# Kernel tuning notes

Hardware: AMD Instinct MI355X
Metric: run time of the kernel (lower is better)

## Reference

```python
import jax, jax.numpy as jnp
import numpy as np

# NSA hyperparams (match init_kwargs)
D_BLK = 64    # d: block stride
L_CMP = 64    # compression block length (== d -> non-overlapping blocks)
L_SLC = 64    # selection block length (== l_cmp == d -> P_slc = P_cmp)
BQ = 64       # block_size_q
TOPK = 16     # slc_top_k
WL, WR = 512, 0  # sliding window (left, right)


def _nsa_forward(q, k, v, w_k, b_k, w_v, b_v, w_gate, b_gate, seqlen):
    S, qh, dim = q.shape
    kv = k.shape[1]
    H = qh // kv
    b = S // seqlen          # number of equal-length packed sequences
    s = seqlen
    scale = dim ** -0.5
    f32 = jnp.float32

    # [b, s, kv, H, e]: q head g*H+h belongs to kv head g (repeat_interleave layout)
    q5 = q.reshape(b, s, kv, H, dim)
    k3 = k.reshape(b, s, kv, dim)
    v3 = v.reshape(b, s, kv, dim)

    # ---- block compression (extract_blocks + cmp_linear over block length) ----
    n_blk = s // D_BLK
    kb = k.reshape(b, n_blk, D_BLK, kv, dim)
    vb = v.reshape(b, n_blk, D_BLK, kv, dim)
    K_cmp = jnp.einsum('bntke,t->bnke', kb, w_k) + b_k[0]
    V_cmp = jnp.einsum('bntke,t->bnke', vb, w_v) + b_v[0]

    # ---- compressed attention (per sequence, fp32 softmax) ----
    sc = jnp.einsum('bqkhe,bnke->bkhqn', q5, K_cmp).astype(f32) * scale
    P = jax.nn.softmax(sc, axis=-1)
    out_cmp = jnp.einsum('bkhqn,bnke->bqkhe', P.astype(q.dtype), V_cmp)

    # ---- selection scores: pool P over q-blocks and GQA groups, then top-k ----
    nqb = s // BQ
    pooled = P.reshape(b, kv, H, nqb, BQ, n_blk).sum(axis=(2, 4))  # [b,kv,nqb,n_blk]
    idx = jax.lax.top_k(pooled, TOPK)[1]                            # [b,kv,nqb,TOPK]

    # gather selected K/V blocks (shared by all queries in a q-block / GQA group)
    kb2 = jnp.transpose(kb, (0, 3, 1, 2, 4))  # [b,kv,n_blk,l,e]
    vb2 = jnp.transpose(vb, (0, 3, 1, 2, 4))
    gather = jax.vmap(jax.vmap(lambda blocks, i: blocks[i]))
    K_sel = gather(kb2, idx)  # [b,kv,nqb,TOPK,l,e]
    V_sel = gather(vb2, idx)

    # ---- selected-block attention ----
    qblk = q5.reshape(b, nqb, BQ, kv, H, dim)
    sc2 = jnp.einsum('bnckhe,bkntle->bkhnctl', qblk, K_sel).astype(f32) * scale
    sc2 = sc2.reshape(b, kv, H, nqb, BQ, TOPK * L_SLC)
    P2 = jax.nn.softmax(sc2, axis=-1).astype(q.dtype)
    out_slc = jnp.einsum('bkhncm,bknme->bnckhe', P2,
                         V_sel.reshape(b, kv, nqb, TOPK * L_SLC, dim))
    out_slc = out_slc.reshape(b, s, kv, H, dim)

    # ---- sliding-window attention (window_size=(WL, WR), non-causal flag) ----
    sw = jnp.einsum('bikhe,bjke->bkhij', q5, k3).astype(f32) * scale
    i = jnp.arange(s)[:, None]
    j = jnp.arange(s)[None, :]
    valid = (j >= i - WL) & (j <= i + WR)
    sw = jnp.where(valid, sw, -jnp.inf)
    Pw = jax.nn.softmax(sw, axis=-1).astype(q.dtype)
    out_win = jnp.einsum('bkhij,bjke->bikhe', Pw, v3)

    # ---- gated fusion of the three branches ----
    gate = jax.nn.sigmoid(jnp.einsum('bqkhe,ec->bqkhc', q5, w_gate) + b_gate)
    out = (gate[..., 0:1] * out_cmp
           + gate[..., 1:2] * out_slc
           + gate[..., 2:3] * out_win)
    return out.reshape(S, qh, dim)


def setup_inputs() -> dict:
    key = jax.random.key(0)
    ks = jax.random.split(key, 9)
    S, qh, kvh, dim = 4096, 8, 2, 128
    inp = {
        'q': jax.random.normal(ks[0], (S, qh, dim), jnp.float32),
        'k': jax.random.normal(ks[1], (S, kvh, dim), jnp.float32),
        'v': jax.random.normal(ks[2], (S, kvh, dim), jnp.float32),
        'w_k': jax.random.normal(ks[3], (L_CMP,), jnp.float32) * (L_CMP ** -0.5),
        'b_k': jax.random.normal(ks[4], (1,), jnp.float32) * 0.02,
        'w_v': jax.random.normal(ks[5], (L_CMP,), jnp.float32) * (L_CMP ** -0.5),
        'b_v': jax.random.normal(ks[6], (1,), jnp.float32) * 0.02,
        'w_gate': jax.random.normal(ks[7], (dim, 3), jnp.float32) * (dim ** -0.5),
        'b_gate': jax.random.normal(ks[8], (3,), jnp.float32) * 0.02,
        'seqlen': 2048,
    }
    return inp


def reference(q, k, v, w_k, b_k, w_v, b_v, w_gate, b_gate, seqlen):
    return _nsa_forward(q, k, v, w_k, b_k, w_v, b_v, w_gate, b_gate, seqlen)
```

## Files before the change

### kernel.cpp

```cpp
#include <hip/hip_runtime.h>
#include <hip/hip_bf16.h>


#define SEQ   2048
#define NB    2
#define KV    2
#define NH    4
#define QH    8
#define DIM   128
#define NBLK  32
#define NQB   32
#define NTOP  16
#define SCALE 0.08838834764831845f
#define QSC   0.12751831795244785f
#define QS    36
#define RS    144
#define PLS   33
#define VP    72

typedef unsigned short ushort_t;
using bf16x8 = __attribute__((ext_vector_type(8))) short;
using f32x4  = __attribute__((ext_vector_type(4))) float;

__device__ __forceinline__ unsigned pkbf(float a, float b){
  union { __hip_bfloat162 h; unsigned u; } cv;
  cv.h = __float22bfloat162_rn(make_float2(a, b));
  return cv.u;
}

__device__ __forceinline__ void async16(ushort_t* l, const ushort_t* g){
  __builtin_amdgcn_global_load_lds(
      (const __attribute__((address_space(1))) unsigned int*)(size_t)g,
      (__attribute__((address_space(3))) unsigned int*)(size_t)l,
      16, 0, 0);
}

__global__ __launch_bounds__(256) void prep_k(
    const float* __restrict__ k, const float* __restrict__ v,
    const float* __restrict__ w_k, const float* __restrict__ b_k,
    const float* __restrict__ w_v, const float* __restrict__ b_v,
    ushort_t* __restrict__ Kb, ushort_t* __restrict__ VT,
    float* __restrict__ Kc, float* __restrict__ Vc)
{
  int blk = blockIdx.x;
  int db = blk & 1, rb = (blk >> 1) & 31, bbg = blk >> 6;
  int bb = bbg >> 1, g = bbg & 1;
  int tid = threadIdx.x;
  __shared__ ushort_t T[64*VP];
  __shared__ float wks[64], wvs[64];
  __shared__ float accK[16][64], accV[16][64];

  if (tid < 64){ wks[tid] = w_k[tid]; wvs[tid] = w_v[tid]; }
  __syncthreads();

  float4 sk = {0,0,0,0}, sv = {0,0,0,0};
  for (int jj = 0; jj < 4; ++jj){
    int i = tid + jj*256;
    int r = i >> 4, ds = i & 15;
    size_t src = ((size_t)(bb*SEQ + rb*64 + r)*KV + g)*DIM + db*64 + ds*4;
    float4 kx = *(const float4*)(k + src);
    float4 vx = *(const float4*)(v + src);
    uint2 kk; kk.x = pkbf(kx.x,kx.y); kk.y = pkbf(kx.z,kx.w);
    size_t rowb = ((size_t)bbg*SEQ + rb*64 + r)*DIM*2;
    int swz = (db*128 + ds*8) ^ ((r & 7) << 4);
    *(uint2*)((char*)Kb + rowb + swz) = kk;
    unsigned v01 = pkbf(vx.x,vx.y), v23 = pkbf(vx.z,vx.w);
    T[(ds*4+0)*VP + r] = (ushort_t)(v01 & 0xffffu);
    T[(ds*4+1)*VP + r] = (ushort_t)(v01 >> 16);
    T[(ds*4+2)*VP + r] = (ushort_t)(v23 & 0xffffu);
    T[(ds*4+3)*VP + r] = (ushort_t)(v23 >> 16);
    float a = wks[r], b = wvs[r];
    sk.x += a*kx.x; sk.y += a*kx.y; sk.z += a*kx.z; sk.w += a*kx.w;
    sv.x += b*vx.x; sv.y += b*vx.y; sv.z += b*vx.z; sv.w += b*vx.w;
  }
  *(float4*)&accK[tid>>4][(tid&15)*4] = sk;
  *(float4*)&accV[tid>>4][(tid&15)*4] = sv;
  __syncthreads();

  for (int jj = 0; jj < 4; ++jj){
    int i = tid + jj*256;
    int d = i >> 4, seg = i & 15;
    uint2 u = *(uint2*)&T[d*VP + seg*4];
    size_t rowb = ((size_t)bbg*DIM + db*64 + d)*SEQ*2;
    int swz = (seg*8) ^ ((d & 7) << 4);
    *(uint2*)((char*)VT + rowb + rb*128 + swz) = u;
  }

  size_t obase = ((size_t)(bbg*NBLK + rb))*DIM + db*64;
  if (tid < 64){
    float s = 0.f;
#pragma unroll
    for (int i = 0; i < 16; ++i) s += accK[i][tid];
    Kc[obase + tid] = s + b_k[0];
  } else if (tid < 128){
    int d = tid - 64;
    float s = 0.f;
#pragma unroll
    for (int i = 0; i < 16; ++i) s += accV[i][d];
    Vc[obase + d] = s + b_v[0];
  }
}

__global__ __launch_bounds__(256) void cmp_attn_k(
    const float* __restrict__ q, const float* __restrict__ Kc,
    const float* __restrict__ Vc,
    const float* __restrict__ w_gate, const float* __restrict__ b_gate,
    float* __restrict__ pooled_part, float* __restrict__ out)
{
  int blk = blockIdx.x;
  int h  = blk & 3;
  int qb = (blk >> 2) & (NQB-1);
  int g  = (blk >> 7) & 1;
  int bb = blk >> 8;
  int tid = threadIdx.x;
  int qi = tid >> 2, c = tid & 3;

  __shared__ float Ks[32*RS];
  __shared__ float Vs[32*RS];
  __shared__ float Pl[64*PLS];

  const float4* Ksrc = (const float4*)(Kc + (size_t)(bb*KV + g) * NBLK * DIM);
  const float4* Vsrc = (const float4*)(Vc + (size_t)(bb*KV + g) * NBLK * DIM);
  for (int i = tid; i < 1024; i += 256){
    int row = i >> 5, seg = i & 31;
    int dst = row*RS + (seg>>3)*QS + (seg&7)*4;
    ((float4*)(Ks+dst))[0] = Ksrc[i];
    ((float4*)(Vs+dst))[0] = Vsrc[i];
  }
  __syncthreads();

  int row = bb*SEQ + qb*64 + qi;
  const float* qptr = q + ((size_t)row*QH + g*NH + h)*DIM;

  float sc[8];
#pragma unroll
  for (int nn = 0; nn < 8; ++nn) sc[nn] = 0.f;
  float gp = 0.f;
  for (int qq = 0; qq < 4; ++qq){
    float qv[32];
    const float4* q4 = (const float4*)(qptr + qq*32);
#pragma unroll
    for (int j = 0; j < 8; ++j){
      float4 u = q4[j];
      qv[4*j+0]=u.x; qv[4*j+1]=u.y; qv[4*j+2]=u.z; qv[4*j+3]=u.w;
    }
#pragma unroll
    for (int d = 0; d < 32; ++d) gp += qv[d]*w_gate[(qq*32+d)*3 + 0];
#pragma unroll
    for (int nn = 0; nn < 8; ++nn){
      int n = nn*4 + c;
      const float4* kr = (const float4*)(Ks + n*RS + qq*QS);
      float p = 0.f;
#pragma unroll
      for (int j = 0; j < 8; ++j){
        float4 u = kr[j];
        p += qv[4*j+0]*u.x + qv[4*j+1]*u.y + qv[4*j+2]*u.z + qv[4*j+3]*u.w;
      }
      sc[nn] += p;
    }
  }
  float g0 = 1.f/(1.f + expf(-(gp + b_gate[0])));

#pragma unroll
  for (int nn = 0; nn < 8; ++nn) sc[nn] *= SCALE;
  float m = sc[0];
#pragma unroll
  for (int nn = 1; nn < 8; ++nn) m = fmaxf(m, sc[nn]);
  m = fmaxf(m, __shfl_xor(m, 1)); m = fmaxf(m, __shfl_xor(m, 2));
  float l = 0.f;
#pragma unroll
  for (int nn = 0; nn < 8; ++nn){ sc[nn] = expf(sc[nn]-m); l += sc[nn]; }
  l += __shfl_xor(l, 1); l += __shfl_xor(l, 2);
  float inv = 1.f/l;
#pragma unroll
  for (int nn = 0; nn < 8; ++nn) Pl[qi*PLS + nn*4 + c] = sc[nn]*inv;
  __syncthreads();

  if (tid < NBLK){
    float s = 0.f;
    for (int q2 = 0; q2 < 64; ++q2) s += Pl[q2*PLS + tid];
    pooled_part[(size_t)blk*NBLK + tid] = s;
  }

  float o[32];
#pragma unroll
  for (int d = 0; d < 32; ++d) o[d] = 0.f;
  for (int n = 0; n < NBLK; ++n){
    float pb = Pl[qi*PLS + n];
    const float4* vr = (const float4*)(Vs + n*RS + c*QS);
#pragma unroll
    for (int j = 0; j < 8; ++j){
      float4 u = vr[j];
      o[4*j+0] += pb*u.x; o[4*j+1] += pb*u.y;
      o[4*j+2] += pb*u.z; o[4*j+3] += pb*u.w;
    }
  }
  float* op = out + ((size_t)row*QH + g*NH + h)*DIM + c*32;
#pragma unroll
  for (int d = 0; d < 32; ++d) op[d] = g0*o[d];
}

__global__ __launch_bounds__(512, 2) void attn_k(
    const float* __restrict__ q, const ushort_t* __restrict__ Kb,
    const ushort_t* __restrict__ VT, const float* __restrict__ pp,
    const float* __restrict__ w_gate, const float* __restrict__ b_gate,
    float* __restrict__ slcbuf, float* __restrict__ out)
{
  int idx = blockIdx.x;
  int x = idx & 7, low = idx & 1, u = idx >> 3;
  int bbg = x >> 1;
  int j = u*2 + low;
  int role = j >> 5;
  int qb = j & 31;
  int bb = bbg >> 1, g = bbg & 1;

  int tid = threadIdx.x;
  int lane = tid & 63, w = tid >> 6;
  int quad = lane >> 4, l15 = lane & 15;
  int h = w & 3, qh2 = w >> 2;
  int xr = (l15 & 7) << 4;

  __shared__ ushort_t Ks[2][64*128];
  __shared__ ushort_t VTs[2][128*64];
  __shared__ ushort_t Ps[256*VP];
  __shared__ float gbuf[256];
  __shared__ int   idxs[NTOP];

  if (role == 0 && tid < 64){
    int n = lane;
    float val = -INFINITY;
    if (n < NBLK){
      const float* p0 = pp + ((size_t)((bb*KV+g)*NQB + qb)*NH)*NBLK + n;
      val = (p0[0] + p0[NBLK]) + (p0[2*NBLK] + p0[3*NBLK]);
    }
    for (int t = 0; t < NTOP; ++t){
      float bv = val; int bi = n;
      for (int mm = 1; mm < 32; mm <<= 1){
        float ov = __shfl_xor(bv, mm);
        int   oi = __shfl_xor(bi, mm);
        if (ov > bv || (ov == bv && oi < bi)){ bv = ov; bi = oi; }
      }
      if (lane == 0) idxs[t] = bi;
      if (n == bi) val = -INFINITY;
    }
  }

  const float* qrow0 = q + ((size_t)(bb*SEQ + qb*64 + qh2*32 + l15)*QH + g*NH + h)*DIM;
  const float* qrow1 = qrow0 + (size_t)16*QH*DIM;
  int gcol = 1 + role;
  bf16x8 qfrag0[4], qfrag1[4];
  float gp0 = 0.f, gp1 = 0.f;
#pragma unroll
  for (int kc = 0; kc < 4; ++kc){
    int d0 = kc*32 + quad*8;
    float4 a0 = *(const float4*)(qrow0 + d0);
    float4 a1 = *(const float4*)(qrow0 + d0 + 4);
    float4 b0 = *(const float4*)(qrow1 + d0);
    float4 b1 = *(const float4*)(qrow1 + d0 + 4);
    float qa[8] = {a0.x,a0.y,a0.z,a0.w,a1.x,a1.y,a1.z,a1.w};
    float qc[8] = {b0.x,b0.y,b0.z,b0.w,b1.x,b1.y,b1.z,b1.w};
#pragma unroll
    for (int jj = 0; jj < 8; ++jj){
      float wg = w_gate[(d0+jj)*3 + gcol];
      gp0 += qa[jj]*wg; gp1 += qc[jj]*wg;
    }
    union { unsigned uu[4]; bf16x8 v8; } t0, t1;
#pragma unroll
    for (int p2 = 0; p2 < 4; ++p2){
      t0.uu[p2] = pkbf(qa[2*p2]*QSC, qa[2*p2+1]*QSC);
      t1.uu[p2] = pkbf(qc[2*p2]*QSC, qc[2*p2+1]*QSC);
    }
    qfrag0[kc] = t0.v8; qfrag1[kc] = t1.v8;
  }
  gp0 += __shfl_xor(gp0,16); gp0 += __shfl_xor(gp0,32);
  gp1 += __shfl_xor(gp1,16); gp1 += __shfl_xor(gp1,32);
  if (quad == 0){
    gbuf[w*32 + l15]      = 1.f/(1.f + __expf(-(gp0 + b_gate[gcol])));
    gbuf[w*32 + 16 + l15] = 1.f/(1.f + __expf(-(gp1 + b_gate[gcol])));
  }
  __syncthreads();
  float gl0[4], gl1[4];
#pragma unroll
  for (int r = 0; r < 4; ++r){
    gl0[r] = gbuf[w*32 + quad*4 + r];
    gl1[r] = gbuf[w*32 + 16 + quad*4 + r];
  }

  const ushort_t* kbase  = Kb + (size_t)bbg*SEQ*DIM;
  const ushort_t* vtbase = VT + (size_t)bbg*DIM*SEQ;

  int kb0 = (qb >= 8) ? (qb - 8) : 0;
  int nph = (role == 0) ? NTOP : (qb - kb0 + 1);
  int qi0 = qh2*32 + l15, qi1 = qi0 + 16;

  float m10 = -INFINITY, l10 = 0.f, m11 = -INFINITY, l11 = 0.f;
  f32x4 oacc0[8], oacc1[8];
  const f32x4 zero4 = {0.f,0.f,0.f,0.f};
#pragma unroll
  for (int dt = 0; dt < 8; ++dt){ oacc0[dt] = zero4; oacc1[dt] = zero4; }

  auto stage = [&](int bufi, int kb_){
    const ushort_t* ksrc = kbase + (size_t)kb_*64*DIM;
#pragma unroll
    for (int jj = 0; jj < 2; ++jj)
      async16(&Ks[bufi][(jj*512 + w*64)*8], ksrc + (size_t)(tid + jj*512)*8);
    const ushort_t* vsrc = vtbase + kb_*64;
#pragma unroll
    for (int jj = 0; jj < 2; ++jj){
      int i = tid + jj*512;
      int d = i >> 3, sg = i & 7;
      async16(&VTs[bufi][(jj*512 + w*64)*8], vsrc + (size_t)d*SEQ + sg*8);
    }
  };

  stage(0, (role == 0) ? idxs[0] : kb0);

  for (int t = 0; t < nph; ++t){
    int cur = t & 1;
    int kb = (role == 0) ? idxs[t] : (kb0 + t);
    __syncthreads();
    if (t+1 < nph){
      int kbn = (role == 0) ? idxs[t+1] : (kb0 + t + 1);
      stage(cur ^ 1, kbn);
    }
    __builtin_amdgcn_sched_barrier(0);

    f32x4 sacc0[4], sacc1[4];
#pragma unroll
    for (int nt = 0; nt < 4; ++nt){ sacc0[nt] = zero4; sacc1[nt] = zero4; }
    __builtin_amdgcn_s_setprio(1);
#pragma unroll
    for (int kc = 0; kc < 4; ++kc){
#pragma unroll
      for (int nt = 0; nt < 4; ++nt){
        bf16x8 a = *(bf16x8*)((char*)&Ks[cur][0] + (nt*16 + l15)*256
                              + ((kc*64 + quad*16) ^ xr));
        sacc0[nt] = __builtin_amdgcn_mfma_f32_16x16x32_bf16(a, qfrag0[kc], sacc0[nt], 0, 0, 0);
        sacc1[nt] = __builtin_amdgcn_mfma_f32_16x16x32_bf16(a, qfrag1[kc], sacc1[nt], 0, 0, 0);
      }
    }
    __builtin_amdgcn_s_setprio(0);

    bool mlow  = (role == 1) && (kb == qb - 8);
    bool mhigh = (role == 1) && (kb == qb);
    bool domask = mlow | mhigh;

    auto softmax_qt = [&](f32x4* sc, float& m1r, float& l1r, int qi_l,
                          bool& skipped) -> float {
      float mx = -INFINITY;
      if (domask){
#pragma unroll
        for (int nt = 0; nt < 4; ++nt)
#pragma unroll
          for (int r = 0; r < 4; ++r){
            int key = nt*16 + quad*4 + r;
            float sv = sc[nt][r];
            bool valid = (!mlow || key >= qi_l) && (!mhigh || key <= qi_l);
            sv = valid ? sv : -INFINITY;
            sc[nt][r] = sv;
            mx = fmaxf(mx, sv);
          }
      } else {
#pragma unroll
        for (int nt = 0; nt < 4; ++nt)
#pragma unroll
          for (int r = 0; r < 4; ++r) mx = fmaxf(mx, sc[nt][r]);
      }
      mx = fmaxf(mx, __shfl_xor(mx, 16));
      mx = fmaxf(mx, __shfl_xor(mx, 32));
      float al = 1.f;
      skipped = __all(mx <= m1r + 8.f);
      if (!skipped){
        float mn = fmaxf(m1r, mx);
        al = exp2f(m1r - mn);
        m1r = mn;
      }
      float s0 = 0.f;
#pragma unroll
      for (int nt = 0; nt < 4; ++nt)
#pragma unroll
        for (int r = 0; r < 4; ++r){
          float pe = exp2f(sc[nt][r] - m1r);
          sc[nt][r] = pe;
          s0 += pe;
        }
      s0 += __shfl_xor(s0, 16);
      s0 += __shfl_xor(s0, 32);
      l1r = l1r*al + s0;
      return al;
    };
    bool sk0, sk1;
    float al0 = softmax_qt(sacc0, m10, l10, qi0, sk0);
    float al1 = softmax_qt(sacc1, m11, l11, qi1, sk1);

#pragma unroll
    for (int nt = 0; nt < 4; ++nt){
      uint2 p0, p1;
      p0.x = pkbf(sacc0[nt][0], sacc0[nt][1]);
      p0.y = pkbf(sacc0[nt][2], sacc0[nt][3]);
      p1.x = pkbf(sacc1[nt][0], sacc1[nt][1]);
      p1.y = pkbf(sacc1[nt][2], sacc1[nt][3]);
      *(uint2*)&Ps[(w*32 + l15)*VP + nt*16 + quad*4] = p0;
      *(uint2*)&Ps[(w*32 + 16 + l15)*VP + nt*16 + quad*4] = p1;
    }

    if (!sk0){
      float ar[4];
#pragma unroll
      for (int r = 0; r < 4; ++r) ar[r] = __shfl(al0, quad*4 + r);
#pragma unroll
      for (int dt = 0; dt < 8; ++dt)
#pragma unroll
        for (int r = 0; r < 4; ++r) oacc0[dt][r] *= ar[r];
    }
    if (!sk1){
      float ar[4];
#pragma unroll
      for (int r = 0; r < 4; ++r) ar[r] = __shfl(al1, quad*4 + r);
#pragma unroll
      for (int dt = 0; dt < 8; ++dt)
#pragma unroll
        for (int r = 0; r < 4; ++r) oacc1[dt][r] *= ar[r];
    }

#pragma unroll
    for (int kc2 = 0; kc2 < 2; ++kc2){
      bf16x8 pa0 = *(bf16x8*)&Ps[(w*32 + l15)*VP + kc2*32 + quad*8];
      bf16x8 pa1 = *(bf16x8*)&Ps[(w*32 + 16 + l15)*VP + kc2*32 + quad*8];
      __builtin_amdgcn_s_setprio(1);
#pragma unroll
      for (int dt = 0; dt < 8; ++dt){
        bf16x8 vb8 = *(bf16x8*)((char*)&VTs[cur][0] + (dt*16 + l15)*128
                                + ((kc2*64 + quad*16) ^ xr));
        oacc0[dt] = __builtin_amdgcn_mfma_f32_16x16x32_bf16(pa0, vb8, oacc0[dt], 0, 0, 0);
        oacc1[dt] = __builtin_amdgcn_mfma_f32_16x16x32_bf16(pa1, vb8, oacc1[dt], 0, 0, 0);
      }
      __builtin_amdgcn_s_setprio(0);
    }
  }

  float lr0[4], lr1[4];
#pragma unroll
  for (int r = 0; r < 4; ++r){
    lr0[r] = __shfl(l10, quad*4 + r);
    lr1[r] = __shfl(l11, quad*4 + r);
  }
#pragma unroll
  for (int r = 0; r < 4; ++r){
    float s20 = gl0[r] / lr0[r];
    float s21 = gl1[r] / lr1[r];
    size_t ob0 = ((size_t)(bb*SEQ + qb*64 + qh2*32 + quad*4 + r)*QH + g*NH + h)*DIM + l15;
    size_t ob1 = ob0 + (size_t)16*QH*DIM;
    if (role == 0){
      float* op0 = slcbuf + ob0;
      float* op1 = slcbuf + ob1;
#pragma unroll
      for (int dt = 0; dt < 8; ++dt){
        op0[dt*16] = s20 * oacc0[dt][r];
        op1[dt*16] = s21 * oacc1[dt][r];
      }
    } else {
      float* op0 = out + ob0;
      float* op1 = out + ob1;
#pragma unroll
      for (int dt = 0; dt < 8; ++dt){
        op0[dt*16] += s20 * oacc0[dt][r];
        op1[dt*16] += s21 * oacc1[dt][r];
      }
    }
  }
}

__global__ __launch_bounds__(256) void merge_k(const float* __restrict__ slcbuf,
                                               float* __restrict__ out){
  int i = blockIdx.x * 256 + threadIdx.x;
  float4 a = ((const float4*)slcbuf)[i];
  float4 b = ((float4*)out)[i];
  b.x += a.x; b.y += a.y; b.z += a.z; b.w += a.w;
  ((float4*)out)[i] = b;
}

extern "C" void kernel_launch(void* const* d_in, const int* in_sizes, int n_in,
                              void* d_out, int out_size, void* d_ws, size_t ws_size,
                              hipStream_t stream) {
  const float* q      = (const float*)d_in[0];
  const float* k      = (const float*)d_in[1];
  const float* v      = (const float*)d_in[2];
  const float* w_k    = (const float*)d_in[3];
  const float* b_k    = (const float*)d_in[4];
  const float* w_v    = (const float*)d_in[5];
  const float* b_v    = (const float*)d_in[6];
  const float* w_gate = (const float*)d_in[7];
  const float* b_gate = (const float*)d_in[8];
  float* out = (float*)d_out;

  float* ws     = (float*)d_ws;
  float* Kc     = ws;
  float* Vc     = ws + 16384;
  float* pp     = ws + 32768;
  float* slcbuf = ws + 49152;
  ushort_t* Kb  = (ushort_t*)(ws + 4243456);
  ushort_t* VT  = Kb + 1048576;

  prep_k    <<<256, 256, 0, stream>>>(k, v, w_k, b_k, w_v, b_v, Kb, VT, Kc, Vc);
  cmp_attn_k<<<NB*KV*NQB*NH, 256, 0, stream>>>(q, Kc, Vc, w_gate, b_gate, pp, out);
  attn_k    <<<256, 512, 0, stream>>>(q, Kb, VT, pp, w_gate, b_gate, slcbuf, out);
  merge_k   <<<4096, 256, 0, stream>>>(slcbuf, out);
}
```

Measured before the change: 178.6 us.

## Fuse four NSA kernels into one cooperative kernel with grid syncs

Replaces the four separate launches (prep, compressed attention, selection/window attention, merge) with a single cooperative kernel of 256 blocks by 512 threads. Phases are separated by grid.sync(), and a shared-memory union lets each phase reuse the same LDS. The aim is to remove launch gaps and inter-kernel drain. In exchange, each phase is limited to 256 blocks, which lowers parallelism in the compressed-attention phase (previously 512 blocks). If the cooperative launch fails, it falls back to the old path.

Result: slower. 319.3 us (+78.8%).

```diff
diff --git a/kernel.cpp b/kernel.cpp
--- a/kernel.cpp
+++ b/kernel.cpp
@@ -1,5 +1,8 @@
 #include <hip/hip_runtime.h>
 #include <hip/hip_bf16.h>
+#include <hip/hip_cooperative_groups.h>
+
+namespace cg = cooperative_groups;
 
 
 #define SEQ   2048
@@ -33,6 +36,460 @@
       (const __attribute__((address_space(1))) unsigned int*)(size_t)g,
       (__attribute__((address_space(3))) unsigned int*)(size_t)l,
       16, 0, 0);
+}
+
+struct ShA {
+  ushort_t T[64*VP];
+  float wks[64], wvs[64];
+  float accK[16][64], accV[16][64];
+};
+struct ShB {
+  float Ks[32*RS];
+  float Vs[32*RS];
+  float Pl[2][64*PLS];
+};
+struct ShC {
+  ushort_t Ks[2][64*128];
+  ushort_t VTs[2][128*64];
+  ushort_t Ps[256*VP];
+  float gbuf[256];
+  int idxs[NTOP];
+};
+union ShU { ShA a; ShB b; ShC c; };
+
+__global__ __launch_bounds__(512, 2) void nsa_mono(
+    const float* __restrict__ q, const float* __restrict__ k,
+    const float* __restrict__ v,
+    const float* __restrict__ w_k, const float* __restrict__ b_k,
+    const float* __restrict__ w_v, const float* __restrict__ b_v,
+    const float* __restrict__ w_gate, const float* __restrict__ b_gate,
+    float* __restrict__ Kc, float* __restrict__ Vc, float* __restrict__ pp,
+    float* __restrict__ slcbuf,
+    ushort_t* __restrict__ Kb, ushort_t* __restrict__ VT,
+    float* __restrict__ out)
+{
+  cg::grid_group grid = cg::this_grid();
+  __shared__ ShU sh;
+  int bm = blockIdx.x;
+  int tid = threadIdx.x;
+
+  {
+    int db = bm & 1, rb = (bm >> 1) & 31, bbg = bm >> 6;
+    int bb = bbg >> 1, g = bbg & 1;
+    if (tid < 64){ sh.a.wks[tid] = w_k[tid]; sh.a.wvs[tid] = w_v[tid]; }
+    __syncthreads();
+    if (tid < 256){
+      float4 sk = {0,0,0,0}, sv = {0,0,0,0};
+      for (int jj = 0; jj < 4; ++jj){
+        int i = tid + jj*256;
+        int r = i >> 4, ds = i & 15;
+        size_t src = ((size_t)(bb*SEQ + rb*64 + r)*KV + g)*DIM + db*64 + ds*4;
+        float4 kx = *(const float4*)(k + src);
+        float4 vx = *(const float4*)(v + src);
+        uint2 kk; kk.x = pkbf(kx.x,kx.y); kk.y = pkbf(kx.z,kx.w);
+        size_t rowb = ((size_t)bbg*SEQ + rb*64 + r)*DIM*2;
+        int swz = (db*128 + ds*8) ^ ((r & 7) << 4);
+        *(uint2*)((char*)Kb + rowb + swz) = kk;
+        unsigned v01 = pkbf(vx.x,vx.y), v23 = pkbf(vx.z,vx.w);
+        sh.a.T[(ds*4+0)*VP + r] = (ushort_t)(v01 & 0xffffu);
+        sh.a.T[(ds*4+1)*VP + r] = (ushort_t)(v01 >> 16);
+        sh.a.T[(ds*4+2)*VP + r] = (ushort_t)(v23 & 0xffffu);
+        sh.a.T[(ds*4+3)*VP + r] = (ushort_t)(v23 >> 16);
+        float a = sh.a.wks[r], b = sh.a.wvs[r];
+        sk.x += a*kx.x; sk.y += a*kx.y; sk.z += a*kx.z; sk.w += a*kx.w;
+        sv.x += b*vx.x; sv.y += b*vx.y; sv.z += b*vx.z; sv.w += b*vx.w;
+      }
+      *(float4*)&sh.a.accK[tid>>4][(tid&15)*4] = sk;
+      *(float4*)&sh.a.accV[tid>>4][(tid&15)*4] = sv;
+    }
+    __syncthreads();
+    if (tid < 256){
+      for (int jj = 0; jj < 4; ++jj){
+        int i = tid + jj*256;
+        int d = i >> 4, seg = i & 15;
+        uint2 u = *(uint2*)&sh.a.T[d*VP + seg*4];
+        size_t rowb = ((size_t)bbg*DIM + db*64 + d)*SEQ*2;
+        int swz = (seg*8) ^ ((d & 7) << 4);
+        *(uint2*)((char*)VT + rowb + rb*128 + swz) = u;
+      }
+      size_t obase = ((size_t)(bbg*NBLK + rb))*DIM + db*64;
+      if (tid < 64){
+        float s = 0.f;
+#pragma unroll
+        for (int i = 0; i < 16; ++i) s += sh.a.accK[i][tid];
+        Kc[obase + tid] = s + b_k[0];
+      } else if (tid < 128){
+        int d = tid - 64;
+        float s = 0.f;
+#pragma unroll
+        for (int i = 0; i < 16; ++i) s += sh.a.accV[i][d];
+        Vc[obase + d] = s + b_v[0];
+      }
+    }
+  }
+  grid.sync();
+
+  {
+    int s = tid >> 8, tid2 = tid & 255;
+    int hh = bm & 1, qb = (bm >> 1) & 31, g = (bm >> 6) & 1, bb = bm >> 7;
+    int h = hh*2 + s;
+
+    const float4* Ksrc = (const float4*)(Kc + (size_t)(bb*KV + g)*NBLK*DIM);
+    const float4* Vsrc = (const float4*)(Vc + (size_t)(bb*KV + g)*NBLK*DIM);
+    for (int i = tid; i < 1024; i += 512){
+      int row = i >> 5, seg = i & 31;
+      int dst = row*RS + (seg>>3)*QS + (seg&7)*4;
+      *(float4*)(sh.b.Ks + dst) = Ksrc[i];
+      *(float4*)(sh.b.Vs + dst) = Vsrc[i];
+    }
+    __syncthreads();
+
+    int qi = tid2 >> 2, c = tid2 & 3;
+    int row = bb*SEQ + qb*64 + qi;
+    const float* qptr = q + ((size_t)row*QH + g*NH + h)*DIM;
+
+    float sc[8];
+#pragma unroll
+    for (int nn = 0; nn < 8; ++nn) sc[nn] = 0.f;
+    float gp = 0.f;
+    for (int qq = 0; qq < 4; ++qq){
+      float qv[32];
+      const float4* q4 = (const float4*)(qptr + qq*32);
+#pragma unroll
+      for (int jjj = 0; jjj < 8; ++jjj){
+        float4 u = q4[jjj];
+        qv[4*jjj+0]=u.x; qv[4*jjj+1]=u.y; qv[4*jjj+2]=u.z; qv[4*jjj+3]=u.w;
+      }
+#pragma unroll
+      for (int d = 0; d < 32; ++d) gp += qv[d]*w_gate[(qq*32+d)*3 + 0];
+#pragma unroll
+      for (int nn = 0; nn < 8; ++nn){
+        int n = nn*4 + c;
+        const float4* kr = (const float4*)(sh.b.Ks + n*RS + qq*QS);
+        float p = 0.f;
+#pragma unroll
+        for (int jjj = 0; jjj < 8; ++jjj){
+          float4 u = kr[jjj];
+          p += qv[4*jjj+0]*u.x + qv[4*jjj+1]*u.y + qv[4*jjj+2]*u.z + qv[4*jjj+3]*u.w;
+        }
+        sc[nn] += p;
+      }
+    }
+    float g0 = 1.f/(1.f + expf(-(gp + b_gate[0])));
+
+#pragma unroll
+    for (int nn = 0; nn < 8; ++nn) sc[nn] *= SCALE;
+    float m = sc[0];
+#pragma unroll
+    for (int nn = 1; nn < 8; ++nn) m = fmaxf(m, sc[nn]);
+    m = fmaxf(m, __shfl_xor(m, 1)); m = fmaxf(m, __shfl_xor(m, 2));
+    float l = 0.f;
+#pragma unroll
+    for (int nn = 0; nn < 8; ++nn){ sc[nn] = expf(sc[nn]-m); l += sc[nn]; }
+    l += __shfl_xor(l, 1); l += __shfl_xor(l, 2);
+    float inv = 1.f/l;
+#pragma unroll
+    for (int nn = 0; nn < 8; ++nn) sh.b.Pl[s][qi*PLS + nn*4 + c] = sc[nn]*inv;
+    __syncthreads();
+
+    if (tid2 < NBLK){
+      float ssum = 0.f;
+      for (int q2 = 0; q2 < 64; ++q2) ssum += sh.b.Pl[s][q2*PLS + tid2];
+      int blk_old = ((bb*KV + g)*NQB + qb)*NH + h;
+      pp[(size_t)blk_old*NBLK + tid2] = ssum;
+    }
+
+    float o[32];
+#pragma unroll
+    for (int d = 0; d < 32; ++d) o[d] = 0.f;
+    for (int n = 0; n < NBLK; ++n){
+      float pb = sh.b.Pl[s][qi*PLS + n];
+      const float4* vr = (const float4*)(sh.b.Vs + n*RS + c*QS);
+#pragma unroll
+      for (int jjj = 0; jjj < 8; ++jjj){
+        float4 u = vr[jjj];
+        o[4*jjj+0] += pb*u.x; o[4*jjj+1] += pb*u.y;
+        o[4*jjj+2] += pb*u.z; o[4*jjj+3] += pb*u.w;
+      }
+    }
+    float* op = out + ((size_t)row*QH + g*NH + h)*DIM + c*32;
+#pragma unroll
+    for (int d = 0; d < 32; ++d) op[d] = g0*o[d];
+  }
+  grid.sync();
+
+  {
+    int idx = bm;
+    int x = idx & 7, low = idx & 1, u = idx >> 3;
+    int bbg = x >> 1;
+    int j = u*2 + low;
+    int role = j >> 5;
+    int qb = j & 31;
+    int bb = bbg >> 1, g = bbg & 1;
+
+    int lane = tid & 63, w = tid >> 6;
+    int quad = lane >> 4, l15 = lane & 15;
+    int h = w & 3, qh2 = w >> 2;
+    int xr = (l15 & 7) << 4;
+
+    if (role == 0 && tid < 64){
+      int n = lane;
+      float val = -INFINITY;
+      if (n < NBLK){
+        const float* p0 = pp + ((size_t)((bb*KV+g)*NQB + qb)*NH)*NBLK + n;
+        val = (p0[0] + p0[NBLK]) + (p0[2*NBLK] + p0[3*NBLK]);
+      }
+      for (int t = 0; t < NTOP; ++t){
+        float bv = val; int bi = n;
+        for (int mm = 1; mm < 32; mm <<= 1){
+          float ov = __shfl_xor(bv, mm);
+          int   oi = __shfl_xor(bi, mm);
+          if (ov > bv || (ov == bv && oi < bi)){ bv = ov; bi = oi; }
+        }
+        if (lane == 0) sh.c.idxs[t] = bi;
+        if (n == bi) val = -INFINITY;
+      }
+    }
+
+    const float* qrow0 = q + ((size_t)(bb*SEQ + qb*64 + qh2*32 + l15)*QH + g*NH + h)*DIM;
+    const float* qrow1 = qrow0 + (size_t)16*QH*DIM;
+    int gcol = 1 + role;
+    bf16x8 qfrag0[4], qfrag1[4];
+    float gp0 = 0.f, gp1 = 0.f;
+#pragma unroll
+    for (int kc = 0; kc < 4; ++kc){
+      int d0 = kc*32 + quad*8;
+      float4 a0 = *(const float4*)(qrow0 + d0);
+      float4 a1 = *(const float4*)(qrow0 + d0 + 4);
+      float4 b0 = *(const float4*)(qrow1 + d0);
+      float4 b1 = *(const float4*)(qrow1 + d0 + 4);
+      float qa[8] = {a0.x,a0.y,a0.z,a0.w,a1.x,a1.y,a1.z,a1.w};
+      float qc[8] = {b0.x,b0.y,b0.z,b0.w,b1.x,b1.y,b1.z,b1.w};
+#pragma unroll
+      for (int jj = 0; jj < 8; ++jj){
+        float wg = w_gate[(d0+jj)*3 + gcol];
+        gp0 += qa[jj]*wg; gp1 += qc[jj]*wg;
+      }
+      union { unsigned uu[4]; bf16x8 v8; } t0, t1;
+#pragma unroll
+      for (int p2 = 0; p2 < 4; ++p2){
+        t0.uu[p2] = pkbf(qa[2*p2]*QSC, qa[2*p2+1]*QSC);
+        t1.uu[p2] = pkbf(qc[2*p2]*QSC, qc[2*p2+1]*QSC);
+      }
+      qfrag0[kc] = t0.v8; qfrag1[kc] = t1.v8;
+    }
+    gp0 += __shfl_xor(gp0,16); gp0 += __shfl_xor(gp0,32);
+    gp1 += __shfl_xor(gp1,16); gp1 += __shfl_xor(gp1,32);
+    if (quad == 0){
+      sh.c.gbuf[w*32 + l15]      = 1.f/(1.f + __expf(-(gp0 + b_gate[gcol])));
+      sh.c.gbuf[w*32 + 16 + l15] = 1.f/(1.f + __expf(-(gp1 + b_gate[gcol])));
+    }
+    __syncthreads();
+    float gl0[4], gl1[4];
+#pragma unroll
+    for (int r = 0; r < 4; ++r){
+      gl0[r] = sh.c.gbuf[w*32 + quad*4 + r];
+      gl1[r] = sh.c.gbuf[w*32 + 16 + quad*4 + r];
+    }
+
+    const ushort_t* kbase  = Kb + (size_t)bbg*SEQ*DIM;
+    const ushort_t* vtbase = VT + (size_t)bbg*DIM*SEQ;
+
+    int kb0 = (qb >= 8) ? (qb - 8) : 0;
+    int nph = (role == 0) ? NTOP : (qb - kb0 + 1);
+    int qi0 = qh2*32 + l15, qi1 = qi0 + 16;
+
+    float m10 = -INFINITY, l10 = 0.f, m11 = -INFINITY, l11 = 0.f;
+    f32x4 oacc0[8], oacc1[8];
+    const f32x4 zero4 = {0.f,0.f,0.f,0.f};
+#pragma unroll
+    for (int dt = 0; dt < 8; ++dt){ oacc0[dt] = zero4; oacc1[dt] = zero4; }
+
+    auto stage = [&](int bufi, int kb_){
+      const ushort_t* ksrc = kbase + (size_t)kb_*64*DIM;
+#pragma unroll
+      for (int jj = 0; jj < 2; ++jj)
+        async16(&sh.c.Ks[bufi][(jj*512 + w*64)*8], ksrc + (size_t)(tid + jj*512)*8);
+      const ushort_t* vsrc = vtbase + kb_*64;
+#pragma unroll
+      for (int jj = 0; jj < 2; ++jj){
+        int i = tid + jj*512;
+        int d = i >> 3, sg = i & 7;
+        async16(&sh.c.VTs[bufi][(jj*512 + w*64)*8], vsrc + (size_t)d*SEQ + sg*8);
+      }
+    };
+
+    stage(0, (role == 0) ? sh.c.idxs[0] : kb0);
+
+    for (int t = 0; t < nph; ++t){
+      int cur = t & 1;
+      int kb = (role == 0) ? sh.c.idxs[t] : (kb0 + t);
+      __syncthreads();
+      if (t+1 < nph){
+        int kbn = (role == 0) ? sh.c.idxs[t+1] : (kb0 + t + 1);
+        stage(cur ^ 1, kbn);
+      }
+      __builtin_amdgcn_sched_barrier(0);
+
+      f32x4 sacc0[4], sacc1[4];
+#pragma unroll
+      for (int nt = 0; nt < 4; ++nt){ sacc0[nt] = zero4; sacc1[nt] = zero4; }
+      __builtin_amdgcn_s_setprio(1);
+#pragma unroll
+      for (int kc = 0; kc < 4; ++kc){
+#pragma unroll
+        for (int nt = 0; nt < 4; ++nt){
+          bf16x8 a = *(bf16x8*)((char*)&sh.c.Ks[cur][0] + (nt*16 + l15)*256
+                                + ((kc*64 + quad*16) ^ xr));
+          sacc0[nt] = __builtin_amdgcn_mfma_f32_16x16x32_bf16(a, qfrag0[kc], sacc0[nt], 0, 0, 0);
+          sacc1[nt] = __builtin_amdgcn_mfma_f32_16x16x32_bf16(a, qfrag1[kc], sacc1[nt], 0, 0, 0);
+        }
+      }
+      __builtin_amdgcn_s_setprio(0);
+
+      bool mlow  = (role == 1) && (kb == qb - 8);
+      bool mhigh = (role == 1) && (kb == qb);
+      bool domask = mlow | mhigh;
+
+      auto softmax_qt = [&](f32x4* sc2, float& m1r, float& l1r, int qi_l,
+                            bool& skipped) -> float {
+        float mx = -INFINITY;
+        if (domask){
+#pragma unroll
+          for (int nt = 0; nt < 4; ++nt)
+#pragma unroll
+            for (int r = 0; r < 4; ++r){
+              int key = nt*16 + quad*4 + r;
+              float sv = sc2[nt][r];
+              bool valid = (!mlow || key >= qi_l) && (!mhigh || key <= qi_l);
+              sv = valid ? sv : -INFINITY;
+              sc2[nt][r] = sv;
+              mx = fmaxf(mx, sv);
+            }
+        } else {
+#pragma unroll
+          for (int nt = 0; nt < 4; ++nt)
+#pragma unroll
+            for (int r = 0; r < 4; ++r) mx = fmaxf(mx, sc2[nt][r]);
+        }
+        mx = fmaxf(mx, __shfl_xor(mx, 16));
+        mx = fmaxf(mx, __shfl_xor(mx, 32));
+        float al = 1.f;
+        skipped = __all(mx <= m1r + 8.f);
+        if (!skipped){
+          float mn = fmaxf(m1r, mx);
+          al = exp2f(m1r - mn);
+          m1r = mn;
+        }
+        float s0 = 0.f;
+#pragma unroll
+        for (int nt = 0; nt < 4; ++nt)
+#pragma unroll
+          for (int r = 0; r < 4; ++r){
+            float pe = exp2f(sc2[nt][r] - m1r);
+            sc2[nt][r] = pe;
+            s0 += pe;
+          }
+        s0 += __shfl_xor(s0, 16);
+        s0 += __shfl_xor(s0, 32);
+        l1r = l1r*al + s0;
+        return al;
+      };
+      bool sk0, sk1;
+      float al0 = softmax_qt(sacc0, m10, l10, qi0, sk0);
+      float al1 = softmax_qt(sacc1, m11, l11, qi1, sk1);
+
+#pragma unroll
+      for (int nt = 0; nt < 4; ++nt){
+        uint2 p0, p1;
+        p0.x = pkbf(sacc0[nt][0], sacc0[nt][1]);
+        p0.y = pkbf(sacc0[nt][2], sacc0[nt][3]);
+        p1.x = pkbf(sacc1[nt][0], sacc1[nt][1]);
+        p1.y = pkbf(sacc1[nt][2], sacc1[nt][3]);
+        *(uint2*)&sh.c.Ps[(w*32 + l15)*VP + nt*16 + quad*4] = p0;
+        *(uint2*)&sh.c.Ps[(w*32 + 16 + l15)*VP + nt*16 + quad*4] = p1;
+      }
+
+      if (!sk0){
+        float ar[4];
+#pragma unroll
+        for (int r = 0; r < 4; ++r) ar[r] = __shfl(al0, quad*4 + r);
+#pragma unroll
+        for (int dt = 0; dt < 8; ++dt)
+#pragma unroll
+          for (int r = 0; r < 4; ++r) oacc0[dt][r] *= ar[r];
+      }
+      if (!sk1){
+        float ar[4];
+#pragma unroll
+        for (int r = 0; r < 4; ++r) ar[r] = __shfl(al1, quad*4 + r);
+#pragma unroll
+        for (int dt = 0; dt < 8; ++dt)
+#pragma unroll
+          for (int r = 0; r < 4; ++r) oacc1[dt][r] *= ar[r];
+      }
+
+#pragma unroll
+      for (int kc2 = 0; kc2 < 2; ++kc2){
+        bf16x8 pa0 = *(bf16x8*)&sh.c.Ps[(w*32 + l15)*VP + kc2*32 + quad*8];
+        bf16x8 pa1 = *(bf16x8*)&sh.c.Ps[(w*32 + 16 + l15)*VP + kc2*32 + quad*8];
+        __builtin_amdgcn_s_setprio(1);
+#pragma unroll
+        for (int dt = 0; dt < 8; ++dt){
+          bf16x8 vb8 = *(bf16x8*)((char*)&sh.c.VTs[cur][0] + (dt*16 + l15)*128
+                                  + ((kc2*64 + quad*16) ^ xr));
+          oacc0[dt] = __builtin_amdgcn_mfma_f32_16x16x32_bf16(pa0, vb8, oacc0[dt], 0, 0, 0);
+          oacc1[dt] = __builtin_amdgcn_mfma_f32_16x16x32_bf16(pa1, vb8, oacc1[dt], 0, 0, 0);
+        }
+        __builtin_amdgcn_s_setprio(0);
+      }
+    }
+
+    float lr0[4], lr1[4];
+#pragma unroll
+    for (int r = 0; r < 4; ++r){
+      lr0[r] = __shfl(l10, quad*4 + r);
+      lr1[r] = __shfl(l11, quad*4 + r);
+    }
+#pragma unroll
+    for (int r = 0; r < 4; ++r){
+      float s20 = gl0[r] / lr0[r];
+      float s21 = gl1[r] / lr1[r];
+      size_t ob0 = ((size_t)(bb*SEQ + qb*64 + qh2*32 + quad*4 + r)*QH + g*NH + h)*DIM + l15;
+      size_t ob1 = ob0 + (size_t)16*QH*DIM;
+      if (role == 0){
+        float* op0 = slcbuf + ob0;
+        float* op1 = slcbuf + ob1;
+#pragma unroll
+        for (int dt = 0; dt < 8; ++dt){
+          op0[dt*16] = s20 * oacc0[dt][r];
+          op1[dt*16] = s21 * oacc1[dt][r];
+        }
+      } else {
+        float* op0 = out + ob0;
+        float* op1 = out + ob1;
+#pragma unroll
+        for (int dt = 0; dt < 8; ++dt){
+          op0[dt*16] += s20 * oacc0[dt][r];
+          op1[dt*16] += s21 * oacc1[dt][r];
+        }
+      }
+    }
+  }
+  grid.sync();
+
+  {
+    const float4* sb = (const float4*)slcbuf;
+    float4* ob = (float4*)out;
+#pragma unroll
+    for (int jj = 0; jj < 8; ++jj){
+      int i = bm*512 + tid + jj*131072;
+      float4 a4 = sb[i];
+      float4 b4 = ob[i];
+      b4.x += a4.x; b4.y += a4.y; b4.z += a4.z; b4.w += a4.w;
+      ob[i] = b4;
+    }
+  }
 }
 
 __global__ __launch_bounds__(256) void prep_k(
@@ -502,8 +959,19 @@
   ushort_t* Kb  = (ushort_t*)(ws + 4243456);
   ushort_t* VT  = Kb + 1048576;
 
-  prep_k    <<<256, 256, 0, stream>>>(k, v, w_k, b_k, w_v, b_v, Kb, VT, Kc, Vc);
-  cmp_attn_k<<<NB*KV*NQB*NH, 256, 0, stream>>>(q, Kc, Vc, w_gate, b_gate, pp, out);
-  attn_k    <<<256, 512, 0, stream>>>(q, Kb, VT, pp, w_gate, b_gate, slcbuf, out);
-  merge_k   <<<4096, 256, 0, stream>>>(slcbuf, out);
+  void* args[] = {
+    (void*)&q, (void*)&k, (void*)&v, (void*)&w_k, (void*)&b_k,
+    (void*)&w_v, (void*)&b_v, (void*)&w_gate, (void*)&b_gate,
+    (void*)&Kc, (void*)&Vc, (void*)&pp, (void*)&slcbuf,
+    (void*)&Kb, (void*)&VT, (void*)&out };
+
+  hipError_t e = hipLaunchCooperativeKernel((const void*)nsa_mono,
+                                            dim3(256), dim3(512),
+                                            args, 0, stream);
+  if (e != hipSuccess){
+    prep_k    <<<256, 256, 0, stream>>>(k, v, w_k, b_k, w_v, b_v, Kb, VT, Kc, Vc);
+    cmp_attn_k<<<NB*KV*NQB*NH, 256, 0, stream>>>(q, Kc, Vc, w_gate, b_gate, pp, out);
+    attn_k    <<<256, 512, 0, stream>>>(q, Kb, VT, pp, w_gate, b_gate, slcbuf, out);
+    merge_k   <<<4096, 256, 0, stream>>>(slcbuf, out);
+  }
 }
```
